# Kernel optimization log

Hardware: AMD Instinct MI355X
Metric: run time of the kernel (lower is better)

The kernel has to match this reference:

```python
import jax, jax.numpy as jnp
import numpy as np

NUM_TRACKS = [128, 256, 512, 1024, 2048, 64, 32, 1024]
B, S, D = 8, 2048, 1536
H = len(NUM_TRACKS)
T = max(NUM_TRACKS)  # num_output_tracks (padded)


def setup_inputs() -> dict:
    key = jax.random.key(0)
    kx, kw, kb, ki = jax.random.split(key, 4)
    x = jax.random.normal(kx, (B, S, D), dtype=jnp.float32)
    # Padded per-species weights: columns >= num_tracks[i] are zero, matching the
    # original's jnp.pad of head logits with zeros.
    track_mask = (jnp.arange(T)[None, :] < jnp.asarray(NUM_TRACKS)[:, None]).astype(jnp.float32)  # [H, T]
    W = jax.random.normal(kw, (H, D, T), dtype=jnp.float32) * 0.02
    W = W * track_mask[:, None, :]
    b = jax.random.normal(kb, (H, T), dtype=jnp.float32) * 0.02
    b = b * track_mask
    head_idx = jax.random.randint(ki, (B,), 0, H, dtype=jnp.int32)
    return {"x": x, "head_idx": head_idx, "W": W, "b": b}


def reference(x, head_idx, W, b):
    # Dense compute of ALL species heads (faithful to original which evaluates
    # every head over the full batch), then per-sample selection via head_idx
    # (equivalent to the original's sequential jnp.where masking).
    logits_all = jnp.einsum('bsd,hdt->bhst', x, W) + b[None, :, None, :]  # [B, H, S, T]
    sel = head_idx[:, None, None, None].astype(jnp.int32)                 # [B, 1, 1, 1]
    logits = jnp.take_along_axis(logits_all, sel, axis=1)[:, 0]           # [B, S, T]
    return logits
```

## Files before the change

kernel.cpp:

```cpp
#include <hip/hip_runtime.h>
#include <hip/hip_bf16.h>
#include <stdint.h>

#define NB 8
#define NS 2048
#define ND 1536
#define NT 2048
#define NH 8
#define NK2 (ND / 64)

__constant__ int c_tiles[NH] = {1, 2, 4, 8, 16, 1, 1, 8};

typedef short bf16x8 __attribute__((ext_vector_type(8)));
typedef unsigned short u16x8 __attribute__((ext_vector_type(8)));
typedef float f32x4 __attribute__((ext_vector_type(4)));

__device__ __forceinline__ unsigned short f2bf(float f) {
    union { float f; unsigned u; } a; a.f = f;
    unsigned r = a.u + 0x7fffu + ((a.u >> 16) & 1u);
    return (unsigned short)(r >> 16);
}

#define XBLK 24576
__global__ void cvt_kernel(const float* __restrict__ x,
                           const float* __restrict__ W,
                           const int* __restrict__ hidx,
                           unsigned short* __restrict__ xb,
                           unsigned short* __restrict__ Wt) {
    const int bid = blockIdx.x;
    const int tid = threadIdx.x;
    if (bid < XBLK) {
        const size_t i = (size_t)bid * 256 + tid;
        float4 v = ((const float4*)x)[i];
        ushort4 o;
        o.x = f2bf(v.x); o.y = f2bf(v.y); o.z = f2bf(v.z); o.w = f2bf(v.w);
        ((ushort4*)xb)[i] = o;
        return;
    }
    const int wid = bid - XBLK;
    const int h = wid / (32 * 24);
    const int rem = wid % (32 * 24);
    const int t0 = (rem % 32) * 64;
    const int d0 = (rem / 32) * 64;
    bool used = false;
    for (int i = 0; i < NB; ++i) used |= (hidx[i] == h);
    if (!used || t0 >= c_tiles[h] * 128) return;

    __shared__ float tile[64][69];
#pragma unroll
    for (int i = 0; i < 4; ++i) {
        const int idx = tid + i * 256;
        const int d = idx >> 4, c = (idx & 15) * 4;
        float4 v = *(const float4*)&W[((size_t)h * ND + d0 + d) * NT + t0 + c];
        tile[d][c] = v.x; tile[d][c + 1] = v.y;
        tile[d][c + 2] = v.z; tile[d][c + 3] = v.w;
    }
    __syncthreads();
    const int t = tid >> 2, dc = (tid & 3) * 16;
    u16x8 o0, o1;
#pragma unroll
    for (int j = 0; j < 8; ++j) o0[j] = f2bf(tile[dc + j][t]);
#pragma unroll
    for (int j = 0; j < 8; ++j) o1[j] = f2bf(tile[dc + 8 + j][t]);
    unsigned short* p = Wt + ((size_t)h * NT + t0 + t) * ND + d0 + dc;
    *(u16x8*)p = o0;
    *(u16x8*)(p + 8) = o1;
}

#define GLDS(g, l)                                                      \
    __builtin_amdgcn_global_load_lds(                                   \
        (const __attribute__((address_space(1))) void*)(g),             \
        (__attribute__((address_space(3))) void*)(l), 16, 0, 0)

#define BAR()                                                           \
    do {                                                                \
        asm volatile("" ::: "memory");                                  \
        __builtin_amdgcn_s_barrier();                                   \
        asm volatile("" ::: "memory");                                  \
    } while (0)
#define WAITV(N) asm volatile("s_waitcnt vmcnt(" #N ")" ::: "memory")

__global__ __launch_bounds__(256) void gemm_kernel(
    const unsigned short* __restrict__ xb,
    const unsigned short* __restrict__ wt,
    const float* __restrict__ bias,
    const int* __restrict__ hidx,
    float* __restrict__ out)
{
    const int tid = threadIdx.x;
    const int id = blockIdx.x;

    int hh[NB], tl[NB];
    int P = 0;
#pragma unroll
    for (int b = 0; b < NB; ++b) {
        hh[b] = hidx[b];
        tl[b] = c_tiles[hh[b]];
        P += tl[b];
    }
    const int C = 16 * P;

    int batch, m0, n0;
    if (id >= C) {
        const int Pz = 128 - P;
        const int z = id - C;
        int p = z % Pz;
        const int m = z / Pz;
        int b = 0;
        while (p >= 16 - tl[b]) { p -= 16 - tl[b]; ++b; }
        batch = b; n0 = (tl[b] + p) * 128; m0 = m * 128;
        float* outb = out + (size_t)batch * NS * NT;
        const int row = tid >> 1;
        const int c0 = (tid & 1) * 64;
        float4 zv = make_float4(0.f, 0.f, 0.f, 0.f);
        float4* ptr = (float4*)(outb + (size_t)(m0 + row) * NT + (n0 + c0));
#pragma unroll
        for (int j = 0; j < 16; ++j) ptr[j] = zv;
        return;
    }
    {
        const int q8 = C >> 3, r8 = C & 7;
        const int xcd = id & 7, i8 = id >> 3;
        const int sid = (xcd < r8 ? xcd * (q8 + 1) : r8 * (q8 + 1) + (xcd - r8) * q8) + i8;
        int p = sid % P;
        const int m = sid / P;
        int b = 0;
        while (p >= tl[b]) { p -= tl[b]; ++b; }
        batch = b; n0 = p * 128; m0 = m * 128;
    }
    const int h = hh[batch];
    float* outb = out + (size_t)batch * NS * NT;

    __shared__ unsigned short As[2][128 * 64];
    __shared__ unsigned short Bs[2][128 * 64];

    const int lane = tid & 63;
    const int wave = tid >> 6;
    const int wm = (wave >> 1) * 64;
    const int wn = (wave & 1) * 64;
    const int fr = lane & 15;
    const int q = lane >> 4;

    const unsigned short* ga[4];
    const unsigned short* gb[4];
    int ca[4], cb[4];
#pragma unroll
    for (int j = 0; j < 4; ++j) {
        const int c = tid + 256 * j;
        const int r = c >> 3, gc = (c & 7) ^ (r & 7);
        ga[j] = xb + ((size_t)batch * NS + m0 + r) * ND + gc * 8;
        ca[j] = c * 8;
        gb[j] = wt + ((size_t)h * NT + n0 + r) * ND + gc * 8;
        cb[j] = c * 8;
    }

    const int sw0 = ((q) ^ (fr & 7)) * 8;
    const int sw1 = ((q + 4) ^ (fr & 7)) * 8;

    f32x4 acc[4][4] = {};

#define PREFETCH(B)                                                   \
    do {                                                              \
        _Pragma("unroll")                                             \
        for (int j = 0; j < 4; ++j) GLDS(ga[j], &As[B][ca[j]]);       \
        _Pragma("unroll")                                             \
        for (int j = 0; j < 4; ++j) GLDS(gb[j], &Bs[B][cb[j]]);       \
        _Pragma("unroll")                                             \
        for (int j = 0; j < 4; ++j) { ga[j] += 64; gb[j] += 64; }     \
    } while (0)

#define COMPUTE(B)                                                            \
    do {                                                                      \
        _Pragma("unroll")                                                     \
        for (int kk = 0; kk < 2; ++kk) {                                      \
            const int sw = kk ? sw1 : sw0;                                    \
            bf16x8 af[4], bfr[4];                                             \
            _Pragma("unroll")                                                 \
            for (int mi = 0; mi < 4; ++mi)                                    \
                af[mi] = *(const bf16x8*)(&As[B][(wm + mi * 16 + fr) * 64 + sw]); \
            _Pragma("unroll")                                                 \
            for (int ni = 0; ni < 4; ++ni)                                    \
                bfr[ni] = *(const bf16x8*)(&Bs[B][(wn + ni * 16 + fr) * 64 + sw]); \
            _Pragma("unroll")                                                 \
            for (int mi = 0; mi < 4; ++mi)                                    \
                _Pragma("unroll")                                             \
                for (int ni = 0; ni < 4; ++ni)                                \
                    acc[mi][ni] = __builtin_amdgcn_mfma_f32_16x16x32_bf16(    \
                        af[mi], bfr[ni], acc[mi][ni], 0, 0, 0);               \
        }                                                                     \
    } while (0)

    PREFETCH(0);
    PREFETCH(1);
    WAITV(8);
    BAR();

    for (int it = 0; it < 11; ++it) {
        COMPUTE(0);
        BAR();
        PREFETCH(0);
        WAITV(8);
        BAR();
        COMPUTE(1);
        BAR();
        PREFETCH(1);
        WAITV(8);
        BAR();
    }
    COMPUTE(0);
    WAITV(0);
    BAR();
    COMPUTE(1);

#undef PREFETCH
#undef COMPUTE

    float bv[4];
#pragma unroll
    for (int ni = 0; ni < 4; ++ni)
        bv[ni] = bias[(size_t)h * NT + n0 + wn + ni * 16 + fr];

    const int rbase = m0 + wm + q * 4;
#pragma unroll
    for (int mi = 0; mi < 4; ++mi) {
#pragma unroll
        for (int r = 0; r < 4; ++r) {
            float* op = outb + (size_t)(rbase + mi * 16 + r) * NT + n0 + wn + fr;
#pragma unroll
            for (int ni = 0; ni < 4; ++ni)
                op[ni * 16] = acc[mi][ni][r] + bv[ni];
        }
    }
}

extern "C" void kernel_launch(void* const* d_in, const int* in_sizes, int n_in,
                              void* d_out, int out_size, void* d_ws, size_t ws_size,
                              hipStream_t stream) {
    const float* x    = (const float*)d_in[0];
    const int*   hidx = (const int*)d_in[1];
    const float* W    = (const float*)d_in[2];
    const float* bias = (const float*)d_in[3];
    float* out = (float*)d_out;

    unsigned short* xb = (unsigned short*)d_ws;
    unsigned short* wt = xb + (size_t)NB * NS * ND;

    cvt_kernel<<<dim3(XBLK + 32 * 24 * NH), dim3(256), 0, stream>>>(
        x, W, hidx, xb, wt);
    gemm_kernel<<<dim3(2048), dim3(256), 0, stream>>>(xb, wt, bias, hidx, out);
}
```

Measured before the change: 328.5 us.

## Load B operand directly from global into registers instead of LDS

Removes the shared-memory staging buffer for the weight tile. Each wave now loads its B fragments straight from global memory into registers, double-buffered alongside the LDS prefetch of A. This cuts LDS traffic and halves LDS usage, which could raise occupancy. In exchange it uses many more VGPRs, each wave re-reads weights that were previously shared across waves, and the global loads are less coalesced. The vmcnt wait thresholds are changed to match the new load count.

```diff
diff --git a/kernel.cpp b/kernel.cpp
--- a/kernel.cpp
+++ b/kernel.cpp
@@ -132,7 +132,6 @@
     float* outb = out + (size_t)batch * NS * NT;
 
     __shared__ unsigned short As[2][128 * 64];
-    __shared__ unsigned short Bs[2][128 * 64];
 
     const int lane = tid & 63;
     const int wave = tid >> 6;
@@ -142,77 +141,87 @@
     const int q = lane >> 4;
 
     const unsigned short* ga[4];
-    const unsigned short* gb[4];
-    int ca[4], cb[4];
+    int ca[4];
 #pragma unroll
     for (int j = 0; j < 4; ++j) {
         const int c = tid + 256 * j;
         const int r = c >> 3, gc = (c & 7) ^ (r & 7);
         ga[j] = xb + ((size_t)batch * NS + m0 + r) * ND + gc * 8;
         ca[j] = c * 8;
-        gb[j] = wt + ((size_t)h * NT + n0 + r) * ND + gc * 8;
-        cb[j] = c * 8;
-    }
+    }
+
+    const unsigned short* gB[4];
+#pragma unroll
+    for (int ni = 0; ni < 4; ++ni)
+        gB[ni] = wt + ((size_t)h * NT + n0 + wn + ni * 16 + fr) * ND + q * 8;
 
     const int sw0 = ((q) ^ (fr & 7)) * 8;
     const int sw1 = ((q + 4) ^ (fr & 7)) * 8;
 
     f32x4 acc[4][4] = {};
-
-#define PREFETCH(B)                                                   \
+    bf16x8 rb0[2][4], rb1[2][4];
+
+#define PREFA(B)                                                      \
     do {                                                              \
         _Pragma("unroll")                                             \
         for (int j = 0; j < 4; ++j) GLDS(ga[j], &As[B][ca[j]]);       \
         _Pragma("unroll")                                             \
-        for (int j = 0; j < 4; ++j) GLDS(gb[j], &Bs[B][cb[j]]);       \
-        _Pragma("unroll")                                             \
-        for (int j = 0; j < 4; ++j) { ga[j] += 64; gb[j] += 64; }     \
-    } while (0)
-
-#define COMPUTE(B)                                                            \
+        for (int j = 0; j < 4; ++j) ga[j] += 64;                      \
+    } while (0)
+
+#define LOADB(R)                                                      \
+    do {                                                              \
+        _Pragma("unroll")                                             \
+        for (int kk = 0; kk < 2; ++kk)                                \
+            _Pragma("unroll")                                         \
+            for (int ni = 0; ni < 4; ++ni)                            \
+                R[kk][ni] = *(const bf16x8*)(gB[ni] + kk * 32);       \
+        _Pragma("unroll")                                             \
+        for (int ni = 0; ni < 4; ++ni) gB[ni] += 64;                  \
+    } while (0)
+
+#define COMPUTE(B, R)                                                         \
     do {                                                                      \
         _Pragma("unroll")                                                     \
         for (int kk = 0; kk < 2; ++kk) {                                      \
             const int sw = kk ? sw1 : sw0;                                    \
-            bf16x8 af[4], bfr[4];                                             \
+            bf16x8 af[4];                                                     \
             _Pragma("unroll")                                                 \
             for (int mi = 0; mi < 4; ++mi)                                    \
                 af[mi] = *(const bf16x8*)(&As[B][(wm + mi * 16 + fr) * 64 + sw]); \
-            _Pragma("unroll")                                                 \
-            for (int ni = 0; ni < 4; ++ni)                                    \
-                bfr[ni] = *(const bf16x8*)(&Bs[B][(wn + ni * 16 + fr) * 64 + sw]); \
             _Pragma("unroll")                                                 \
             for (int mi = 0; mi < 4; ++mi)                                    \
                 _Pragma("unroll")                                             \
                 for (int ni = 0; ni < 4; ++ni)                                \
                     acc[mi][ni] = __builtin_amdgcn_mfma_f32_16x16x32_bf16(    \
-                        af[mi], bfr[ni], acc[mi][ni], 0, 0, 0);               \
+                        af[mi], R[kk][ni], acc[mi][ni], 0, 0, 0);             \
         }                                                                     \
     } while (0)
 
-    PREFETCH(0);
-    PREFETCH(1);
-    WAITV(8);
+    PREFA(0); LOADB(rb0);
+    PREFA(1); LOADB(rb1);
+    WAITV(12);
     BAR();
 
     for (int it = 0; it < 11; ++it) {
-        COMPUTE(0);
-        BAR();
-        PREFETCH(0);
-        WAITV(8);
-        BAR();
-        COMPUTE(1);
-        BAR();
-        PREFETCH(1);
-        WAITV(8);
-        BAR();
-    }
-    COMPUTE(0);
+        COMPUTE(0, rb0);
+        BAR();
+        PREFA(0); LOADB(rb0);
+        WAITV(12);
+        BAR();
+        COMPUTE(1, rb1);
+        BAR();
+        PREFA(1); LOADB(rb1);
+        WAITV(12);
+        BAR();
+    }
+    COMPUTE(0, rb0);
     WAITV(0);
     BAR();
-    COMPUTE(1);
-
-#undef PREFETCH
+    COMPUTE(1, rb1);
+
+#undef PREFA
+#undef LOADB
 #undef COMPUTE
 
     float bv[4];
```

Result: slower. 362.4 us (+10.3%).

## Enlarge GEMM tiles to 256x256 with 512-thread blocks and pad weights

Applied to the files above, without the earlier changes.

The GEMM block tile grows from 128x128 to 256x256, using 8 waves that each compute a 128x64 sub-tile, and the grid shrinks to 512 blocks. This raises reuse of each global/LDS load and cuts per-block scheduling overhead. Because tiles are now 256 columns wide, the weight conversion kernel writes zeros into the padding columns for heads with an odd 128-tile count, so narrow heads now compute on padded data. MFMA sections are also wrapped in s_setprio to favor the math waves. The cost is a doubled LDS footprint, which limits occupancy, plus wasted compute on heads with few tracks.

```diff
diff --git a/kernel.cpp b/kernel.cpp
--- a/kernel.cpp
+++ b/kernel.cpp
@@ -44,7 +44,17 @@
     const int d0 = (rem / 32) * 64;
     bool used = false;
     for (int i = 0; i < NB; ++i) used |= (hidx[i] == h);
-    if (!used || t0 >= c_tiles[h] * 128) return;
+    const int tl = c_tiles[h];
+    const int tl2 = (tl + 1) >> 1;
+    if (!used || t0 >= tl2 * 256) return;
+    if (t0 >= tl * 128) {
+        const int t = tid >> 2, dc = (tid & 3) * 16;
+        u16x8 z = {};
+        unsigned short* p = Wt + ((size_t)h * NT + t0 + t) * ND + d0 + dc;
+        *(u16x8*)p = z;
+        *(u16x8*)(p + 8) = z;
+        return;
+    }
 
     __shared__ float tile[64][69];
 #pragma unroll
@@ -80,7 +90,7 @@
     } while (0)
 #define WAITV(N) asm volatile("s_waitcnt vmcnt(" #N ")" ::: "memory")
 
-__global__ __launch_bounds__(256) void gemm_kernel(
+__global__ __launch_bounds__(512, 2) void gemm_kernel(
     const unsigned short* __restrict__ xb,
     const unsigned short* __restrict__ wt,
     const float* __restrict__ bias,
@@ -90,54 +100,54 @@
     const int tid = threadIdx.x;
     const int id = blockIdx.x;
 
-    int hh[NB], tl[NB];
-    int P = 0;
+    int hh[NB], tl2[NB];
+    int S = 0;
 #pragma unroll
     for (int b = 0; b < NB; ++b) {
         hh[b] = hidx[b];
-        tl[b] = c_tiles[hh[b]];
-        P += tl[b];
-    }
-    const int C = 16 * P;
+        tl2[b] = (c_tiles[hh[b]] + 1) >> 1;
+        S += tl2[b];
+    }
+    const int C = 8 * S;
 
     int batch, m0, n0;
     if (id >= C) {
-        const int Pz = 128 - P;
+        const int Pz = 64 - S;
         const int z = id - C;
         int p = z % Pz;
         const int m = z / Pz;
         int b = 0;
-        while (p >= 16 - tl[b]) { p -= 16 - tl[b]; ++b; }
-        batch = b; n0 = (tl[b] + p) * 128; m0 = m * 128;
+        while (p >= 8 - tl2[b]) { p -= 8 - tl2[b]; ++b; }
+        batch = b; n0 = (tl2[b] + p) * 256; m0 = m * 256;
         float* outb = out + (size_t)batch * NS * NT;
         const int row = tid >> 1;
-        const int c0 = (tid & 1) * 64;
+        const int c0 = (tid & 1) * 128;
         float4 zv = make_float4(0.f, 0.f, 0.f, 0.f);
         float4* ptr = (float4*)(outb + (size_t)(m0 + row) * NT + (n0 + c0));
 #pragma unroll
-        for (int j = 0; j < 16; ++j) ptr[j] = zv;
+        for (int j = 0; j < 32; ++j) ptr[j] = zv;
         return;
     }
     {
         const int q8 = C >> 3, r8 = C & 7;
         const int xcd = id & 7, i8 = id >> 3;
         const int sid = (xcd < r8 ? xcd * (q8 + 1) : r8 * (q8 + 1) + (xcd - r8) * q8) + i8;
-        int p = sid % P;
-        const int m = sid / P;
+        int p = sid % S;
+        const int m = sid / S;
         int b = 0;
-        while (p >= tl[b]) { p -= tl[b]; ++b; }
-        batch = b; n0 = p * 128; m0 = m * 128;
+        while (p >= tl2[b]) { p -= tl2[b]; ++b; }
+        batch = b; n0 = p * 256; m0 = m * 256;
     }
     const int h = hh[batch];
     float* outb = out + (size_t)batch * NS * NT;
 
-    __shared__ unsigned short As[2][128 * 64];
-    __shared__ unsigned short Bs[2][128 * 64];
+    __shared__ unsigned short As[2][256 * 64];
+    __shared__ unsigned short Bs[2][256 * 64];
 
     const int lane = tid & 63;
     const int wave = tid >> 6;
-    const int wm = (wave >> 1) * 64;
-    const int wn = (wave & 1) * 64;
+    const int wm = (wave >> 2) * 128;
+    const int wn = (wave & 3) * 64;
     const int fr = lane & 15;
     const int q = lane >> 4;
 
@@ -146,7 +156,7 @@
     int ca[4], cb[4];
 #pragma unroll
     for (int j = 0; j < 4; ++j) {
-        const int c = tid + 256 * j;
+        const int c = tid + 512 * j;
         const int r = c >> 3, gc = (c & 7) ^ (r & 7);
         ga[j] = xb + ((size_t)batch * NS + m0 + r) * ND + gc * 8;
         ca[j] = c * 8;
@@ -157,7 +167,7 @@
     const int sw0 = ((q) ^ (fr & 7)) * 8;
     const int sw1 = ((q + 4) ^ (fr & 7)) * 8;
 
-    f32x4 acc[4][4] = {};
+    f32x4 acc[8][4] = {};
 
 #define PREFETCH(B)                                                   \
     do {                                                              \
@@ -174,19 +184,21 @@
         _Pragma("unroll")                                                     \
         for (int kk = 0; kk < 2; ++kk) {                                      \
             const int sw = kk ? sw1 : sw0;                                    \
-            bf16x8 af[4], bfr[4];                                             \
+            bf16x8 af[8], bfr[4];                                             \
             _Pragma("unroll")                                                 \
-            for (int mi = 0; mi < 4; ++mi)                                    \
+            for (int mi = 0; mi < 8; ++mi)                                    \
                 af[mi] = *(const bf16x8*)(&As[B][(wm + mi * 16 + fr) * 64 + sw]); \
             _Pragma("unroll")                                                 \
             for (int ni = 0; ni < 4; ++ni)                                    \
                 bfr[ni] = *(const bf16x8*)(&Bs[B][(wn + ni * 16 + fr) * 64 + sw]); \
+            __builtin_amdgcn_s_setprio(1);                                    \
             _Pragma("unroll")                                                 \
-            for (int mi = 0; mi < 4; ++mi)                                    \
+            for (int mi = 0; mi < 8; ++mi)                                    \
                 _Pragma("unroll")                                             \
                 for (int ni = 0; ni < 4; ++ni)                                \
                     acc[mi][ni] = __builtin_amdgcn_mfma_f32_16x16x32_bf16(    \
                         af[mi], bfr[ni], acc[mi][ni], 0, 0, 0);               \
+            __builtin_amdgcn_s_setprio(0);                                    \
         }                                                                     \
     } while (0)
 
@@ -222,7 +234,7 @@
 
     const int rbase = m0 + wm + q * 4;
 #pragma unroll
-    for (int mi = 0; mi < 4; ++mi) {
+    for (int mi = 0; mi < 8; ++mi) {
 #pragma unroll
         for (int r = 0; r < 4; ++r) {
             float* op = outb + (size_t)(rbase + mi * 16 + r) * NT + n0 + wn + fr;
@@ -247,5 +259,5 @@
 
     cvt_kernel<<<dim3(XBLK + 32 * 24 * NH), dim3(256), 0, stream>>>(
         x, W, hidx, xb, wt);
-    gemm_kernel<<<dim3(2048), dim3(256), 0, stream>>>(xb, wt, bias, hidx, out);
-}
+    gemm_kernel<<<dim3(512), dim3(512), 0, stream>>>(xb, wt, bias, hidx, out);
+}
```

Measured after the change: 318.9 us. 2.9% less time.

## Use 256x128 GEMM tiles with 512 threads, triple-buffered LDS and MFMA priority

Applied to the files above, without the earlier changes.

The GEMM block tile grows from 128x128 to 256x128 with 8 waves per block, so each weight tile loaded into LDS feeds twice as many rows, and the grid shrinks to 1024 blocks. The LDS pipeline goes from double to triple buffering, with a deeper prefetch and adjusted vmcnt waits so global loads run further ahead of compute. The MFMA sections are wrapped in s_setprio to favour matrix issue. In exchange, LDS use rises to about 144KB per block, which limits occupancy to one block per CU, and there are fewer blocks to balance across CUs.

```diff
diff --git a/kernel.cpp b/kernel.cpp
--- a/kernel.cpp
+++ b/kernel.cpp
@@ -80,7 +80,7 @@
     } while (0)
 #define WAITV(N) asm volatile("s_waitcnt vmcnt(" #N ")" ::: "memory")
 
-__global__ __launch_bounds__(256) void gemm_kernel(
+__global__ __launch_bounds__(512) void gemm_kernel(
     const unsigned short* __restrict__ xb,
     const unsigned short* __restrict__ wt,
     const float* __restrict__ bias,
@@ -98,7 +98,7 @@
         tl[b] = c_tiles[hh[b]];
         P += tl[b];
     }
-    const int C = 16 * P;
+    const int C = 8 * P;
 
     int batch, m0, n0;
     if (id >= C) {
@@ -108,7 +108,7 @@
         const int m = z / Pz;
         int b = 0;
         while (p >= 16 - tl[b]) { p -= 16 - tl[b]; ++b; }
-        batch = b; n0 = (tl[b] + p) * 128; m0 = m * 128;
+        batch = b; n0 = (tl[b] + p) * 128; m0 = m * 256;
         float* outb = out + (size_t)batch * NS * NT;
         const int row = tid >> 1;
         const int c0 = (tid & 1) * 64;
@@ -126,13 +126,13 @@
         const int m = sid / P;
         int b = 0;
         while (p >= tl[b]) { p -= tl[b]; ++b; }
-        batch = b; n0 = p * 128; m0 = m * 128;
+        batch = b; n0 = p * 128; m0 = m * 256;
     }
     const int h = hh[batch];
     float* outb = out + (size_t)batch * NS * NT;
 
-    __shared__ unsigned short As[2][128 * 64];
-    __shared__ unsigned short Bs[2][128 * 64];
+    __shared__ unsigned short As[3][256 * 64];
+    __shared__ unsigned short Bs[3][128 * 64];
 
     const int lane = tid & 63;
     const int wave = tid >> 6;
@@ -142,14 +142,20 @@
     const int q = lane >> 4;
 
     const unsigned short* ga[4];
-    const unsigned short* gb[4];
-    int ca[4], cb[4];
+    int ca[4];
 #pragma unroll
     for (int j = 0; j < 4; ++j) {
-        const int c = tid + 256 * j;
+        const int c = tid + 512 * j;
         const int r = c >> 3, gc = (c & 7) ^ (r & 7);
         ga[j] = xb + ((size_t)batch * NS + m0 + r) * ND + gc * 8;
         ca[j] = c * 8;
+    }
+    const unsigned short* gb[2];
+    int cb[2];
+#pragma unroll
+    for (int j = 0; j < 2; ++j) {
+        const int c = tid + 512 * j;
+        const int r = c >> 3, gc = (c & 7) ^ (r & 7);
         gb[j] = wt + ((size_t)h * NT + n0 + r) * ND + gc * 8;
         cb[j] = c * 8;
     }
@@ -164,9 +170,11 @@
         _Pragma("unroll")                                             \
         for (int j = 0; j < 4; ++j) GLDS(ga[j], &As[B][ca[j]]);       \
         _Pragma("unroll")                                             \
-        for (int j = 0; j < 4; ++j) GLDS(gb[j], &Bs[B][cb[j]]);       \
-        _Pragma("unroll")                                             \
-        for (int j = 0; j < 4; ++j) { ga[j] += 64; gb[j] += 64; }     \
+        for (int j = 0; j < 2; ++j) GLDS(gb[j], &Bs[B][cb[j]]);       \
+        _Pragma("unroll")                                             \
+        for (int j = 0; j < 4; ++j) ga[j] += 64;                      \
+        _Pragma("unroll")                                             \
+        for (int j = 0; j < 2; ++j) gb[j] += 64;                      \
     } while (0)
 
 #define COMPUTE(B)                                                            \
@@ -181,36 +189,30 @@
             _Pragma("unroll")                                                 \
             for (int ni = 0; ni < 4; ++ni)                                    \
                 bfr[ni] = *(const bf16x8*)(&Bs[B][(wn + ni * 16 + fr) * 64 + sw]); \
+            __builtin_amdgcn_s_setprio(1);                                    \
             _Pragma("unroll")                                                 \
             for (int mi = 0; mi < 4; ++mi)                                    \
                 _Pragma("unroll")                                             \
                 for (int ni = 0; ni < 4; ++ni)                                \
                     acc[mi][ni] = __builtin_amdgcn_mfma_f32_16x16x32_bf16(    \
                         af[mi], bfr[ni], acc[mi][ni], 0, 0, 0);               \
+            __builtin_amdgcn_s_setprio(0);                                    \
         }                                                                     \
     } while (0)
 
     PREFETCH(0);
     PREFETCH(1);
-    WAITV(8);
+    WAITV(6);
     BAR();
 
-    for (int it = 0; it < 11; ++it) {
-        COMPUTE(0);
-        BAR();
-        PREFETCH(0);
-        WAITV(8);
-        BAR();
-        COMPUTE(1);
-        BAR();
-        PREFETCH(1);
-        WAITV(8);
-        BAR();
-    }
-    COMPUTE(0);
-    WAITV(0);
-    BAR();
-    COMPUTE(1);
+    for (int it = 0; it < 7; ++it) {
+        PREFETCH(2); WAITV(12); BAR(); COMPUTE(0); BAR();
+        PREFETCH(0); WAITV(12); BAR(); COMPUTE(1); BAR();
+        PREFETCH(1); WAITV(12); BAR(); COMPUTE(2); BAR();
+    }
+    PREFETCH(2); WAITV(12); BAR(); COMPUTE(0); BAR();
+    WAITV(6); BAR(); COMPUTE(1); BAR();
+    WAITV(0); BAR(); COMPUTE(2);
 
 #undef PREFETCH
 #undef COMPUTE
@@ -247,5 +249,5 @@
 
     cvt_kernel<<<dim3(XBLK + 32 * 24 * NH), dim3(256), 0, stream>>>(
         x, W, hidx, xb, wt);
-    gemm_kernel<<<dim3(2048), dim3(256), 0, stream>>>(xb, wt, bias, hidx, out);
-}
+    gemm_kernel<<<dim3(1024), dim3(512), 0, stream>>>(xb, wt, bias, hidx, out);
+}
```

Measured after the change: 324.9 us. About the same (-1.1%).
